# Optimization experiments

Measured on AMD Instinct MI355X. Metric: run time of the kernel, lower is better.

The kernel has to match this reference:

```python
import jax, jax.numpy as jnp
import numpy as np
from jax import lax


def setup_inputs() -> dict:
    key = jax.random.key(0)
    k1, k2, k3, k4, k5 = jax.random.split(key, 5)
    B, T, D, N = 64, 1024, 512, 24
    return {
        "x": jax.random.normal(k1, (B, T, D), dtype=jnp.float32),
        "W": jax.random.normal(k2, (D, N), dtype=jnp.float32) * 0.05,
        "b": jnp.zeros((N,), dtype=jnp.float32),
        "trans": jax.random.normal(k3, (N, N), dtype=jnp.float32) * 0.1,
        "left_boundary": jax.random.normal(k4, (N,), dtype=jnp.float32) * 0.1,
        "right_boundary": jax.random.normal(k5, (N,), dtype=jnp.float32) * 0.1,
    }


def reference(x, W, b, trans, left_boundary, right_boundary):
    # Dense projection to tag potentials: [B, T, N]
    pot = jnp.einsum("btd,dn->btn", x, W) + b
    B, T, N = pot.shape
    # mask=None -> lengths are all T; boundaries added at t=0 and t=T-1
    lens = jnp.full((B,), T, dtype=jnp.int32)
    pot = pot.at[:, 0, :].add(left_boundary).at[:, T - 1, :].add(right_boundary)

    # Viterbi forward: alpha[b, j] = best score of any path ending in tag j
    def fwd_step(alpha, pot_t):
        scores = alpha[:, :, None] + trans[None, :, :]  # [B, prev, cur]
        bp = jnp.argmax(scores, axis=1)                 # [B, N] best prev tag
        alpha_new = jnp.max(scores, axis=1) + pot_t
        return alpha_new, bp

    alpha0 = pot[:, 0, :]
    pot_rest = jnp.swapaxes(pot[:, 1:, :], 0, 1)  # [T-1, B, N]
    alpha_T, bps = lax.scan(fwd_step, alpha0, pot_rest)
    last_tag = jnp.argmax(alpha_T, axis=-1)  # [B]

    # Backtrack through backpointers (reverse scan over time)
    def back_step(tag, bp_t):
        prev = jnp.take_along_axis(bp_t, tag[:, None], axis=1)[:, 0]
        return prev, prev

    _, tags_head = lax.scan(back_step, last_tag, bps, reverse=True)  # [T-1, B]
    decoded = jnp.concatenate(
        [jnp.swapaxes(tags_head, 0, 1), last_tag[:, None]], axis=1
    ).astype(jnp.int32)  # [B, T]
    return decoded, pot, lens, trans
```

## Files before the change

kernel.cpp:

```cpp
#include <hip/hip_runtime.h>
#include <hip/hip_bf16.h>

#define BB 64
#define TT 1024
#define DD 512
#define NS 24

#define POT_OFF   65536
#define LENS_OFF  1638400
#define TRANS_OFF 1638464

__global__ __launch_bounds__(256) void gemm_pot(
    const float* __restrict__ x, const float* __restrict__ W,
    const float* __restrict__ bias, const float* __restrict__ trans,
    const float* __restrict__ lb, const float* __restrict__ rb,
    float* __restrict__ out)
{
  __shared__ float wl[DD * NS];
  const int tid = threadIdx.x;
  const int l   = tid & 63;
  const int q   = tid >> 6;
  const int row = blockIdx.x * 64 + l;

  {
    const float4* Ws = (const float4*)W;
    float4* Wd = (float4*)wl;
#pragma unroll
    for (int i = 0; i < 12; ++i) Wd[tid + i * 256] = Ws[tid + i * 256];
  }
  __syncthreads();

  const float4* xp = (const float4*)(x + (size_t)row * DD + q * 128);

  float acc[NS];
#pragma unroll
  for (int nn = 0; nn < NS; ++nn) acc[nn] = 0.f;

  float4 buf[8];
#pragma unroll
  for (int i = 0; i < 8; ++i) buf[i] = xp[i];

#pragma unroll
  for (int f = 0; f < 32; ++f) {
    float4 v = buf[f & 7];
    if (f + 8 < 32) buf[f & 7] = xp[f + 8];
    const float xj[4] = {v.x, v.y, v.z, v.w};
#pragma unroll
    for (int j = 0; j < 4; ++j) {
      const int k = q * 128 + f * 4 + j;
      const float4* wr = (const float4*)&wl[k * NS];
      float4 w0 = wr[0], w1 = wr[1], w2 = wr[2], w3 = wr[3], w4 = wr[4], w5 = wr[5];
      const float wv[NS] = {w0.x,w0.y,w0.z,w0.w, w1.x,w1.y,w1.z,w1.w,
                            w2.x,w2.y,w2.z,w2.w, w3.x,w3.y,w3.z,w3.w,
                            w4.x,w4.y,w4.z,w4.w, w5.x,w5.y,w5.z,w5.w};
      const float xv = xj[j];
#pragma unroll
      for (int nn = 0; nn < NS; ++nn) acc[nn] = fmaf(xv, wv[nn], acc[nn]);
    }
  }

  __syncthreads();
  if (q != 0) {
#pragma unroll
    for (int nn = 0; nn < NS; ++nn) wl[((q - 1) * 64 + l) * 25 + nn] = acc[nn];
  }
  __syncthreads();
  if (q == 0) {
    const int t = row & (TT - 1);
#pragma unroll
    for (int nn = 0; nn < NS; ++nn)
      acc[nn] += wl[(0 * 64 + l) * 25 + nn] + wl[(1 * 64 + l) * 25 + nn]
               + wl[(2 * 64 + l) * 25 + nn] + bias[nn];
    if (t == 0) {
#pragma unroll
      for (int nn = 0; nn < NS; ++nn) acc[nn] += lb[nn];
    }
    if (t == TT - 1) {
#pragma unroll
      for (int nn = 0; nn < NS; ++nn) acc[nn] += rb[nn];
    }
    float* po = out + POT_OFF + (size_t)row * NS;
#pragma unroll
    for (int i = 0; i < 6; ++i)
      *(float4*)(po + i * 4) = make_float4(acc[4*i], acc[4*i+1], acc[4*i+2], acc[4*i+3]);
  }

  if (blockIdx.x == 0 && tid < BB) out[LENS_OFF + tid] = (float)TT;
  if (blockIdx.x == 1) {
    for (int i = tid; i < NS * NS; i += 256) out[TRANS_OFF + i] = trans[i];
  }
}

__device__ __forceinline__ float m3(float a, float b, float c) {
  return fmaxf(fmaxf(a, b), c);
}

#define RORI(dst, src, J) \
  dst = __builtin_amdgcn_mov_dpp((src), 0x120 + (J), 0xF, 0xF, true)

__global__ __launch_bounds__(1024) void viterbi_fused(
    const float* __restrict__ pot, const float* __restrict__ trans,
    float* __restrict__ out_dec)
{
  __shared__ float ps[(TT + 8) * NS];
  __shared__ unsigned char bl[TT * NS];
  __shared__ float tl[NS * NS];
  __shared__ int H[32][NS];
  __shared__ int e[32];

  const int b = blockIdx.x, tid = threadIdx.x;

  {
    const float4* src = (const float4*)(pot + (size_t)b * TT * NS);
    float4* dst = (float4*)ps;
#pragma unroll
    for (int i = 0; i < 6; ++i) dst[tid + i * 1024] = src[tid + i * 1024];
    if (tid < NS * NS) tl[tid] = trans[tid];
  }
  __syncthreads();

  if (tid < 64) {
    const int r = tid >> 4;
    const int c = tid & 15;
    const int g = r >> 1;
    const int n = 16 * (r & 1) + c;
    const int nm = (n < NS) ? n : (NS - 1);
    const bool wr = (n < NS) && (g == 0);

    int colv[16];
    colv[0] = c;
    RORI(colv[1],  c, 1);  RORI(colv[2],  c, 2);  RORI(colv[3],  c, 3);
    RORI(colv[4],  c, 4);  RORI(colv[5],  c, 5);  RORI(colv[6],  c, 6);
    RORI(colv[7],  c, 7);  RORI(colv[8],  c, 8);  RORI(colv[9],  c, 9);
    RORI(colv[10], c, 10); RORI(colv[11], c, 11); RORI(colv[12], c, 12);
    RORI(colv[13], c, 13); RORI(colv[14], c, 14); RORI(colv[15], c, 15);

    bool selx;
    {
      auto nr = __builtin_amdgcn_permlane16_swap(n, n, false, false);
      selx = (nr[0] == 16 * g + c);
    }

    float tcr[16];
#pragma unroll
    for (int j = 0; j < 16; ++j) {
      const int m = 16 * g + colv[j];
      tcr[j] = (m < NS) ? tl[m * NS + nm] : -__builtin_inff();
    }

    float ar[16];
#pragma unroll
    for (int j = 0; j < 16; ++j) {
      const int m = 16 * g + colv[j];
      ar[j] = ps[(m < NS) ? m : (NS - 1)];
    }

    float pv[8];
#pragma unroll
    for (int u = 0; u < 8; ++u) pv[u] = ps[(1 + u) * NS + nm];

    auto step = [&](int tt, float potv) {
      float sc[16];
#pragma unroll
      for (int j = 0; j < 16; ++j) sc[j] = ar[j] + tcr[j];
      float u0 = m3(sc[0],  sc[1],  sc[2]);
      float u1 = m3(sc[3],  sc[4],  sc[5]);
      float u2 = m3(sc[6],  sc[7],  sc[8]);
      float u3 = m3(sc[9],  sc[10], sc[11]);
      float u4 = m3(sc[12], sc[13], sc[14]);
      float pm = fmaxf(m3(u0, u1, u2), m3(u3, u4, sc[15]));
      auto pr = __builtin_amdgcn_permlane32_swap(
          __float_as_int(pm), __float_as_int(pm), false, false);
      float al = fmaxf(__int_as_float(pr[0]), __int_as_float(pr[1])) + potv;
      if (wr) ps[tt * NS + n] = al;
      auto qr = __builtin_amdgcn_permlane16_swap(
          __float_as_int(al), __float_as_int(al), false, false);
      int asel = selx ? qr[0] : qr[1];
      ar[0] = __int_as_float(asel);
      int d1, d2, d3, d4, d5, d6, d7, d8, d9, d10, d11, d12, d13, d14, d15;
      RORI(d1,  asel, 1);  ar[1]  = __int_as_float(d1);
      RORI(d2,  asel, 2);  ar[2]  = __int_as_float(d2);
      RORI(d3,  asel, 3);  ar[3]  = __int_as_float(d3);
      RORI(d4,  asel, 4);  ar[4]  = __int_as_float(d4);
      RORI(d5,  asel, 5);  ar[5]  = __int_as_float(d5);
      RORI(d6,  asel, 6);  ar[6]  = __int_as_float(d6);
      RORI(d7,  asel, 7);  ar[7]  = __int_as_float(d7);
      RORI(d8,  asel, 8);  ar[8]  = __int_as_float(d8);
      RORI(d9,  asel, 9);  ar[9]  = __int_as_float(d9);
      RORI(d10, asel, 10); ar[10] = __int_as_float(d10);
      RORI(d11, asel, 11); ar[11] = __int_as_float(d11);
      RORI(d12, asel, 12); ar[12] = __int_as_float(d12);
      RORI(d13, asel, 13); ar[13] = __int_as_float(d13);
      RORI(d14, asel, 14); ar[14] = __int_as_float(d14);
      RORI(d15, asel, 15); ar[15] = __int_as_float(d15);
    };

    for (int t = 1; t + 7 <= TT - 1; t += 8) {
#pragma unroll
      for (int u = 0; u < 8; ++u) {
        const int tt = t + u;
        const float potv = pv[u];
        pv[u] = ps[(tt + 8) * NS + nm];
        step(tt, potv);
      }
    }
#pragma unroll
    for (int u = 0; u < 7; ++u) step(1017 + u, pv[u]);
  }
  __syncthreads();

  for (int idx = tid; idx < (TT - 1) * NS; idx += 1024) {
    const int n = idx % NS;
    const int t = idx / NS + 1;
    const float* ar = &ps[(t - 1) * NS];
    float best = ar[0] + tl[n];
    int bi = 0;
#pragma unroll
    for (int m = 1; m < NS; ++m) {
      float s = ar[m] + tl[m * NS + n];
      bool gg = s > best;
      bi = gg ? m : bi;
      best = gg ? s : best;
    }
    bl[t * NS + n] = (unsigned char)bi;
  }
  __syncthreads();

  if (tid < 32 * NS) {
    const int c2 = tid / NS, s = tid % NS;
    int a2 = s;
    int tlo = c2 * 32; if (tlo < 1) tlo = 1;
    for (int t = c2 * 32 + 31; t >= tlo; --t) a2 = bl[t * NS + a2];
    H[c2][s] = a2;
  }
  __syncthreads();

  if (tid == 0) {
    const float* ar = &ps[(TT - 1) * NS];
    float best = ar[0]; int bi = 0;
#pragma unroll
    for (int nn = 1; nn < NS; ++nn) {
      float v = ar[nn];
      if (v > best) { best = v; bi = nn; }
    }
    int tag = bi;
    e[31] = tag;
    for (int c2 = 31; c2 >= 1; --c2) { tag = H[c2][tag]; e[c2 - 1] = tag; }
  }
  __syncthreads();

  if (tid < 32) {
    const int c2 = tid;
    int tag = e[c2];
    float* od = out_dec + (size_t)b * TT;
    od[c2 * 32 + 31] = (float)tag;
    for (int t = c2 * 32 + 30; t >= c2 * 32; --t) {
      tag = bl[(t + 1) * NS + tag];
      od[t] = (float)tag;
    }
  }
}

extern "C" void kernel_launch(void* const* d_in, const int* in_sizes, int n_in,
                              void* d_out, int out_size, void* d_ws, size_t ws_size,
                              hipStream_t stream)
{
  const float* x     = (const float*)d_in[0];
  const float* W     = (const float*)d_in[1];
  const float* bias  = (const float*)d_in[2];
  const float* trans = (const float*)d_in[3];
  const float* lb    = (const float*)d_in[4];
  const float* rb    = (const float*)d_in[5];
  float* out = (float*)d_out;

  gemm_pot<<<1024, 256, 0, stream>>>(x, W, bias, trans, lb, rb, out);
  viterbi_fused<<<BB, 1024, 0, stream>>>(out + POT_OFF, trans, out);
}
```

Baseline: 327.0 us.

## Compute two rows per thread in GEMM and cache transition column in registers

```diff
diff --git a/kernel.cpp b/kernel.cpp
--- a/kernel.cpp
+++ b/kernel.cpp
@@ -20,7 +20,8 @@
   const int tid = threadIdx.x;
   const int l   = tid & 63;
   const int q   = tid >> 6;
-  const int row = blockIdx.x * 64 + l;
+  const int row0 = blockIdx.x * 128 + l;
+  const int row1 = row0 + 64;
 
   {
     const float4* Ws = (const float4*)W;
@@ -30,21 +31,24 @@
   }
   __syncthreads();
 
-  const float4* xp = (const float4*)(x + (size_t)row * DD + q * 128);
-
-  float acc[NS];
-#pragma unroll
-  for (int nn = 0; nn < NS; ++nn) acc[nn] = 0.f;
-
-  float4 buf[8];
-#pragma unroll
-  for (int i = 0; i < 8; ++i) buf[i] = xp[i];
+  const float4* xp0 = (const float4*)(x + (size_t)row0 * DD + q * 128);
+  const float4* xp1 = (const float4*)(x + (size_t)row1 * DD + q * 128);
+
+  float acc0[NS], acc1[NS];
+#pragma unroll
+  for (int nn = 0; nn < NS; ++nn) { acc0[nn] = 0.f; acc1[nn] = 0.f; }
+
+  float4 buf0[4], buf1[4];
+#pragma unroll
+  for (int i = 0; i < 4; ++i) { buf0[i] = xp0[i]; buf1[i] = xp1[i]; }
 
 #pragma unroll
   for (int f = 0; f < 32; ++f) {
-    float4 v = buf[f & 7];
-    if (f + 8 < 32) buf[f & 7] = xp[f + 8];
-    const float xj[4] = {v.x, v.y, v.z, v.w};
+    float4 v0 = buf0[f & 3];
+    float4 v1 = buf1[f & 3];
+    if (f + 4 < 32) { buf0[f & 3] = xp0[f + 4]; buf1[f & 3] = xp1[f + 4]; }
+    const float xj0[4] = {v0.x, v0.y, v0.z, v0.w};
+    const float xj1[4] = {v1.x, v1.y, v1.z, v1.w};
 #pragma unroll
     for (int j = 0; j < 4; ++j) {
       const int k = q * 128 + f * 4 + j;
@@ -53,36 +57,49 @@
       const float wv[NS] = {w0.x,w0.y,w0.z,w0.w, w1.x,w1.y,w1.z,w1.w,
                             w2.x,w2.y,w2.z,w2.w, w3.x,w3.y,w3.z,w3.w,
                             w4.x,w4.y,w4.z,w4.w, w5.x,w5.y,w5.z,w5.w};
-      const float xv = xj[j];
-#pragma unroll
-      for (int nn = 0; nn < NS; ++nn) acc[nn] = fmaf(xv, wv[nn], acc[nn]);
+      const float xv0 = xj0[j];
+      const float xv1 = xj1[j];
+#pragma unroll
+      for (int nn = 0; nn < NS; ++nn) {
+        acc0[nn] = fmaf(xv0, wv[nn], acc0[nn]);
+        acc1[nn] = fmaf(xv1, wv[nn], acc1[nn]);
+      }
     }
   }
 
   __syncthreads();
   if (q != 0) {
 #pragma unroll
-    for (int nn = 0; nn < NS; ++nn) wl[((q - 1) * 64 + l) * 25 + nn] = acc[nn];
+    for (int nn = 0; nn < NS; ++nn) {
+      wl[((q - 1) * 128 + l)      * 25 + nn] = acc0[nn];
+      wl[((q - 1) * 128 + 64 + l) * 25 + nn] = acc1[nn];
+    }
   }
   __syncthreads();
   if (q == 0) {
-    const int t = row & (TT - 1);
-#pragma unroll
-    for (int nn = 0; nn < NS; ++nn)
-      acc[nn] += wl[(0 * 64 + l) * 25 + nn] + wl[(1 * 64 + l) * 25 + nn]
-               + wl[(2 * 64 + l) * 25 + nn] + bias[nn];
-    if (t == 0) {
-#pragma unroll
-      for (int nn = 0; nn < NS; ++nn) acc[nn] += lb[nn];
-    }
-    if (t == TT - 1) {
-#pragma unroll
-      for (int nn = 0; nn < NS; ++nn) acc[nn] += rb[nn];
-    }
-    float* po = out + POT_OFF + (size_t)row * NS;
-#pragma unroll
-    for (int i = 0; i < 6; ++i)
-      *(float4*)(po + i * 4) = make_float4(acc[4*i], acc[4*i+1], acc[4*i+2], acc[4*i+3]);
+#pragma unroll
+    for (int rr = 0; rr < 2; ++rr) {
+      float* acc = rr ? acc1 : acc0;
+      const int row = rr ? row1 : row0;
+      const int slot = rr ? (64 + l) : l;
+      const int t = row & (TT - 1);
+#pragma unroll
+      for (int nn = 0; nn < NS; ++nn)
+        acc[nn] += wl[(0 * 128 + slot) * 25 + nn] + wl[(1 * 128 + slot) * 25 + nn]
+                 + wl[(2 * 128 + slot) * 25 + nn] + bias[nn];
+      if (t == 0) {
+#pragma unroll
+        for (int nn = 0; nn < NS; ++nn) acc[nn] += lb[nn];
+      }
+      if (t == TT - 1) {
+#pragma unroll
+        for (int nn = 0; nn < NS; ++nn) acc[nn] += rb[nn];
+      }
+      float* po = out + POT_OFF + (size_t)row * NS;
+#pragma unroll
+      for (int i = 0; i < 6; ++i)
+        *(float4*)(po + i * 4) = make_float4(acc[4*i], acc[4*i+1], acc[4*i+2], acc[4*i+3]);
+    }
   }
 
   if (blockIdx.x == 0 && tid < BB) out[LENS_OFF + tid] = (float)TT;
@@ -209,20 +226,31 @@
   }
   __syncthreads();
 
-  for (int idx = tid; idx < (TT - 1) * NS; idx += 1024) {
-    const int n = idx % NS;
-    const int t = idx / NS + 1;
-    const float* ar = &ps[(t - 1) * NS];
-    float best = ar[0] + tl[n];
-    int bi = 0;
-#pragma unroll
-    for (int m = 1; m < NS; ++m) {
-      float s = ar[m] + tl[m * NS + n];
-      bool gg = s > best;
-      bi = gg ? m : bi;
-      best = gg ? s : best;
-    }
-    bl[t * NS + n] = (unsigned char)bi;
+  if (tid < 1008) {
+    const int grp = tid / 24;
+    const int n   = tid - grp * 24;
+    float tlc[NS];
+#pragma unroll
+    for (int m = 0; m < NS; ++m) tlc[m] = tl[m * NS + n];
+    for (int t = 1 + grp; t <= TT - 1; t += 42) {
+      const float4* rr = (const float4*)&ps[(t - 1) * NS];
+      float ar[NS];
+#pragma unroll
+      for (int i = 0; i < 6; ++i) {
+        float4 v = rr[i];
+        ar[4*i] = v.x; ar[4*i+1] = v.y; ar[4*i+2] = v.z; ar[4*i+3] = v.w;
+      }
+      float best = ar[0] + tlc[0];
+      int bi = 0;
+#pragma unroll
+      for (int m = 1; m < NS; ++m) {
+        float s = ar[m] + tlc[m];
+        bool gg = s > best;
+        bi = gg ? m : bi;
+        best = gg ? s : best;
+      }
+      bl[t * NS + n] = (unsigned char)bi;
+    }
   }
   __syncthreads();
 
@@ -273,6 +301,6 @@
   const float* rb    = (const float*)d_in[5];
   float* out = (float*)d_out;
 
-  gemm_pot<<<1024, 256, 0, stream>>>(x, W, bias, trans, lb, rb, out);
+  gemm_pot<<<512, 256, 0, stream>>>(x, W, bias, trans, lb, rb, out);
   viterbi_fused<<<BB, 1024, 0, stream>>>(out + POT_OFF, trans, out);
 }
```

Result: no change. 321.7 us (-1.6%).
